# Kernel optimization log

Hardware: AMD Instinct MI355X
Metric: run time of the kernel (lower is better)

Reference implementation:

```python
import jax, jax.numpy as jnp
import numpy as np

B, S = 4, 8192
DIM, H = 1024, 8
C = 2 * H           # num_channels
E = DIM // C        # head_dim = 64
BASE, START, STRIDE = 10.0, 0, 1
CHUNK = 64
EPS = 1e-8
TWO_PI = 2.0 * np.pi


def setup_inputs() -> dict:
    key = jax.random.key(0)
    k1, k2, k3, k4, k5 = jax.random.split(key, 5)
    inputs = jax.random.normal(k1, (B, S, DIM), jnp.float32)
    timestamps = jnp.sort(jax.random.randint(k2, (B, S), 0, 8192, jnp.int32), axis=-1)
    next_timestamps = jnp.sort(jax.random.randint(k3, (B, S), 0, 8192, jnp.int32), axis=-1)
    mask = jnp.ones((B, S), dtype=bool)
    # learned parameters
    Wv = jax.random.normal(k4, (DIM, DIM), jnp.float32) / np.sqrt(DIM)  # proj_v.weight
    gamma_param = jnp.zeros((H,), jnp.float32)
    alpha = jax.random.normal(k5, (C,), jnp.float32) * 0.02
    beta = jnp.ones((C,), jnp.float32)
    return {"inputs": inputs, "Wv": Wv, "gamma_param": gamma_param, "alpha": alpha,
            "beta": beta, "timestamps": timestamps, "next_timestamps": next_timestamps,
            "mask": mask}


def chunkwise_recurrent_attention(q, k, v, decay_steps, mask, chunk):
    # q,k: [B,S,C,2]; v: [B,S,C,E]; decay_steps: [B,S,C]; mask: [B,S] bool
    b, s, c, d = q.shape
    e = v.shape[-1]
    m4 = mask[..., None, None].astype(q.dtype)
    q = q * m4
    k = k * m4
    v = v * m4
    decay = jnp.where(mask[..., None], decay_steps, jnp.ones_like(decay_steps))
    n = s // chunk

    def chunks(x):  # [B,S,...] -> [n,B,L,...]
        return x.reshape(b, n, chunk, *x.shape[2:]).swapaxes(0, 1)

    qc, kc, vc = chunks(q), chunks(k), chunks(v)
    dc = chunks(decay)                       # [n,B,L,C]
    mc = mask.reshape(b, n, chunk).swapaxes(0, 1)
    causal = jnp.tril(jnp.ones((chunk, chunk), q.dtype))

    def step(state, xs):
        qch, kch, vch, dch, mch = xs         # [B,L,C,2],[B,L,C,2],[B,L,C,E],[B,L,C],[B,L]
        prefix = jnp.cumprod(jnp.clip(dch, EPS), axis=1)            # [B,L,C]
        prev = jnp.einsum('blcd,bcde->blce', qch * prefix[..., None], state)
        dmat = prefix[:, :, None, :] / jnp.clip(prefix[:, None, :, :], EPS)  # [B,L,M,C]
        scores = jnp.einsum('blcd,bmcd->blmc', qch, kch)            # [B,L,M,C]
        weights = scores * dmat * causal[None, :, :, None]
        intra = jnp.einsum('blmc,bmce->blce', weights, vch)
        out = (prev + intra) * mch[..., None, None].astype(qch.dtype)
        plast = prefix[:, -1]                                       # [B,C]
        sw = plast[:, None, :] / jnp.clip(prefix, EPS)              # [B,L,C]
        new_state = state * plast[:, :, None, None] + \
            jnp.einsum('blcd,blce->bcde', kch * sw[..., None], vch)
        return new_state, out

    state0 = jnp.zeros((b, c, d, e), q.dtype)
    _, outs = jax.lax.scan(step, state0, (qc, kc, vc, dc, mc))
    return outs.swapaxes(0, 1).reshape(b, s, c, e)


def _forward(inputs, Wv, gamma_param, alpha, beta, timestamps, next_timestamps, mask):
    values = (inputs @ Wv.T).reshape(B, S, C, E)
    scales = jnp.arange(START, START + H * STRIDE, STRIDE, dtype=jnp.float32)
    intervals = jnp.power(BASE, scales).astype(jnp.int32).astype(jnp.float32)  # buffer cast to long
    scale_factor = TWO_PI * jnp.power(1.0 / BASE, scales)
    ts = timestamps.astype(jnp.float32)
    nts = next_timestamps.astype(jnp.float32)
    theta_k = jnp.remainder(ts[..., None], intervals) * scale_factor   # [B,S,H]
    theta_q = jnp.remainder(nts[..., None], intervals) * scale_factor
    key_ = jnp.stack((jnp.cos(theta_k), jnp.sin(theta_k)), axis=-1)    # [B,S,H,2]
    key_ = jnp.concatenate([key_, key_], axis=2)                       # [B,S,C,2]
    cos_q, sin_q = jnp.cos(theta_q), jnp.sin(theta_q)
    query = jnp.concatenate([jnp.stack((sin_q, -cos_q), -1),
                             jnp.stack((cos_q, sin_q), -1)], axis=2)   # [B,S,C,2]
    gamma = jax.nn.sigmoid(gamma_param)
    loggamma = jnp.log(jnp.clip(gamma, 1e-6))
    delta = jnp.clip(nts - ts, 0.0)
    q_decay = jnp.exp(loggamma * (delta[..., None] * scale_factor))    # [B,S,H]
    q_decay = jnp.concatenate([q_decay, q_decay], axis=-1)             # [B,S,C]
    query = query * q_decay[..., None]
    step_delta = jnp.concatenate(
        [jnp.zeros((B, 1), jnp.float32), jnp.clip(ts[:, 1:] - ts[:, :-1], 0.0)], axis=1)
    decay_steps = jnp.exp(loggamma * (step_delta[..., None] * scale_factor))
    decay_steps = jnp.concatenate([decay_steps, decay_steps], axis=-1)  # [B,S,C]
    out = chunkwise_recurrent_attention(query, key_, values, decay_steps, mask, CHUNK)
    out = out * alpha[None, None, :, None] + values * beta[None, None, :, None]
    return out.reshape(B, S, DIM)


def reference(inputs, Wv, gamma_param, alpha, beta, timestamps, next_timestamps, mask):
    return _forward(inputs, Wv, gamma_param, alpha, beta, timestamps, next_timestamps, mask)
```

## Files before the change

kernel.cpp:

```cpp
#include <hip/hip_runtime.h>
#include <stdint.h>

#define SS   8192
#define DIMD 1024
#define NCH  128
#define CC   16
#define EPSF 1e-8f

typedef __bf16 bh;
typedef bh    bhx4 __attribute__((ext_vector_type(4)));
typedef bh    bhx8 __attribute__((ext_vector_type(8)));
typedef float fx4  __attribute__((ext_vector_type(4)));
typedef unsigned int u32x2 __attribute__((ext_vector_type(2)));

#define GLOAD_LDS16(g, l) __builtin_amdgcn_global_load_lds(                    \
    (const __attribute__((address_space(1))) uint32_t*)(g),                    \
    (__attribute__((address_space(3))) uint32_t*)(l), 16, 0, 0)

#define LDSA(p) ((uint32_t)(uintptr_t)(const __attribute__((address_space(3))) char*)(const char*)(p))

#define SB() __builtin_amdgcn_sched_barrier(0)
#define PRE_BAR()  do { SB(); __builtin_amdgcn_s_barrier(); SB();              \
                        __builtin_amdgcn_s_setprio(1); } while (0)
#define POST_BAR() do { __builtin_amdgcn_s_setprio(0); SB();                   \
                        __builtin_amdgcn_s_barrier(); SB(); } while (0)

__global__ __launch_bounds__(256) void cvt_k(const float* __restrict__ src,
                                             bh* __restrict__ dst, int n8) {
    int i = blockIdx.x * 256 + threadIdx.x;
    if (i >= n8) return;
    const float4 a = reinterpret_cast<const float4*>(src)[i * 2];
    const float4 b = reinterpret_cast<const float4*>(src)[i * 2 + 1];
    bhx8 o;
    o[0] = (bh)a.x; o[1] = (bh)a.y; o[2] = (bh)a.z; o[3] = (bh)a.w;
    o[4] = (bh)b.x; o[5] = (bh)b.y; o[6] = (bh)b.z; o[7] = (bh)b.w;
    reinterpret_cast<bhx8*>(dst)[i] = o;
}

template <typename VT>
__global__ __launch_bounds__(512, 2) void gemm256a(const bh* __restrict__ A,
                                                   const bh* __restrict__ Bw,
                                                   VT* __restrict__ C,
                                                   const int* __restrict__ tsp,
                                                   const float* __restrict__ gammap,
                                                   float* __restrict__ Aws,
                                                   float* __restrict__ plastWs) {
    __shared__ __align__(16) char ldsraw[131072];
    const int lb = blockIdx.x;
    const int logical = (lb & 7) * 64 + (lb >> 3);
    const int mt = logical >> 2;
    const int nt = logical & 3;
    const int tid = threadIdx.x, lane = tid & 63, w = tid >> 6;
    const int wm = w >> 2, wn = w & 3;

    fx4 acc[8][4];
#pragma unroll
    for (int i = 0; i < 8; ++i)
#pragma unroll
        for (int j = 0; j < 4; ++j)
#pragma unroll
            for (int r = 0; r < 4; ++r) acc[i][j][r] = 0.f;

    const int kgo = ((tid & 3) ^ ((tid >> 3) & 3)) << 3;
    const bh* gA0 = A  + (size_t)(mt * 256 + (tid >> 2)) * DIMD + kgo;
    const bh* gB0 = Bw + (size_t)(nt * 256 + (tid >> 2)) * DIMD + kgo;

#define STAGE_U(kt, obase, g, h)                                               \
    { char* lp = ldsraw + ((((kt) & 1) * 65536) + (obase) + (h) * 16384) + tid * 16; \
      const bh* gp = (g) + (kt) * 64 + (h) * 32;                               \
      GLOAD_LDS16(gp, lp);                                                     \
      GLOAD_LDS16(gp + 131072, lp + 8192); }

    const int rAb = wm * 128 + (lane & 15);
    const int rBb = wn * 64 + (lane & 15);
    const int s_swz = (lane >> 4) ^ (((lane & 15) >> 1) & 3);
    const int offA = rAb * 64 + s_swz * 16;
    const int offB = rBb * 64 + s_swz * 16;

    STAGE_U(0, 0, gA0, 0); STAGE_U(0, 32768, gB0, 0);
    STAGE_U(0, 0, gA0, 1); STAGE_U(0, 32768, gB0, 1);
    STAGE_U(1, 0, gA0, 0); STAGE_U(1, 32768, gB0, 0);
    STAGE_U(1, 0, gA0, 1); STAGE_U(1, 32768, gB0, 1);
    asm volatile("s_waitcnt vmcnt(8)" ::: "memory");
    SB(); __builtin_amdgcn_s_barrier(); SB();

#pragma unroll 2
    for (int t = 0; t < 16; ++t) {
        const int buf = t & 1;
        const char* pA0 = ldsraw + buf * 65536 + offA;
        const char* pB0 = ldsraw + buf * 65536 + 32768 + offB;
        bhx8 fa[4], fb[4];

#pragma unroll
        for (int i = 0; i < 4; ++i) fa[i] = *reinterpret_cast<const bhx8*>(pA0 + i * 1024);
#pragma unroll
        for (int j = 0; j < 4; ++j) fb[j] = *reinterpret_cast<const bhx8*>(pB0 + j * 1024);
        if (t >= 1 && t <= 14) STAGE_U(t + 1, 0, gA0, 1);
        PRE_BAR();
#pragma unroll
        for (int i = 0; i < 4; ++i)
#pragma unroll
            for (int j = 0; j < 4; ++j)
                acc[i][j] = __builtin_amdgcn_mfma_f32_16x16x32_bf16(fa[i], fb[j], acc[i][j], 0, 0, 0);
        POST_BAR();

#pragma unroll
        for (int i = 0; i < 4; ++i) fa[i] = *reinterpret_cast<const bhx8*>(pA0 + (4 + i) * 1024);
        if (t <= 13) STAGE_U(t + 2, 32768, gB0, 0);
        PRE_BAR();
#pragma unroll
        for (int i = 0; i < 4; ++i)
#pragma unroll
            for (int j = 0; j < 4; ++j)
                acc[4 + i][j] = __builtin_amdgcn_mfma_f32_16x16x32_bf16(fa[i], fb[j], acc[4 + i][j], 0, 0, 0);
        POST_BAR();

#pragma unroll
        for (int i = 0; i < 4; ++i) fa[i] = *reinterpret_cast<const bhx8*>(pA0 + 16384 + i * 1024);
#pragma unroll
        for (int j = 0; j < 4; ++j) fb[j] = *reinterpret_cast<const bhx8*>(pB0 + 16384 + j * 1024);
        if (t <= 13) STAGE_U(t + 2, 0, gA0, 0);
        PRE_BAR();
#pragma unroll
        for (int i = 0; i < 4; ++i)
#pragma unroll
            for (int j = 0; j < 4; ++j)
                acc[i][j] = __builtin_amdgcn_mfma_f32_16x16x32_bf16(fa[i], fb[j], acc[i][j], 0, 0, 0);
        POST_BAR();

#pragma unroll
        for (int i = 0; i < 4; ++i) fa[i] = *reinterpret_cast<const bhx8*>(pA0 + 16384 + (4 + i) * 1024);
        if (t <= 13) STAGE_U(t + 2, 32768, gB0, 1);
        PRE_BAR();
#pragma unroll
        for (int i = 0; i < 4; ++i)
#pragma unroll
            for (int j = 0; j < 4; ++j)
                acc[4 + i][j] = __builtin_amdgcn_mfma_f32_16x16x32_bf16(fa[i], fb[j], acc[4 + i][j], 0, 0, 0);
        __builtin_amdgcn_s_setprio(0);
        if (t < 14)       { asm volatile("s_waitcnt vmcnt(6)" ::: "memory"); }
        else if (t == 14) { asm volatile("s_waitcnt vmcnt(0)" ::: "memory"); }
        SB(); __builtin_amdgcn_s_barrier(); SB();
    }
#undef STAGE_U

    const int r0 = (lane >> 4) * 4;
    const int c0 = lane & 15;
#pragma unroll
    for (int mi = 0; mi < 8; ++mi) {
#pragma unroll
        for (int ni = 0; ni < 4; ++ni) {
            const size_t m = (size_t)(mt * 256 + wm * 128 + mi * 16 + r0);
            const int    n = nt * 256 + wn * 64 + ni * 16 + c0;
#pragma unroll
            for (int r = 0; r < 4; ++r) {
                if constexpr (sizeof(VT) == 2)
                    C[(m + r) * DIMD + n] = (bh)acc[mi][ni][r];
                else
                    C[(m + r) * DIMD + n] = acc[mi][ni][r];
            }
        }
    }

    float* wlds = (float*)ldsraw + w * 256;
    const int b_ = mt >> 5;
    const int j0 = (mt & 31) * 4;
    const int c_ = nt * 4 + wn;
    const int h_ = c_ & 7;
    float iv = 1.f; double invb = 1.0;
    for (int i = 0; i < h_; i++) { iv *= 10.f; invb *= 0.1; }
    const float sf = (float)(6.283185307179586 * invb);
    const float gm = 1.f / (1.f + expf(-gammap[h_]));
    const float lg = logf(fmaxf(gm, 1e-6f));

#pragma unroll
    for (int jl = 0; jl < 2; ++jl) {
        const int jg = j0 + wm * 2 + jl;
        const int sl = jg * 64 + lane;
        const int its = tsp[b_ * SS + sl];
        const int itp = (sl > 0) ? tsp[b_ * SS + sl - 1] : its;
        int dstep = its - itp; if (dstep < 0) dstep = 0;
        const float dec = expf(lg * ((float)dstep * sf));
        float p = fmaxf(dec, EPSF);
#pragma unroll
        for (int off = 1; off < 64; off <<= 1) {
            float o = __shfl_up(p, off, 64);
            if (lane >= off) p *= o;
        }
        const float plast = __shfl(p, 63, 64);
        const float swv = plast / fmaxf(p, EPSF);
        const float tk = fmodf((float)its, iv) * sf;
        wlds[jl * 128 + lane]      = cosf(tk) * swv;
        wlds[jl * 128 + 64 + lane] = sinf(tk) * swv;
        if (lane == 0) plastWs[(size_t)(b_ * CC + c_) * NCH + jg] = plast;
    }
    asm volatile("s_waitcnt lgkmcnt(0)" ::: "memory");

#pragma unroll
    for (int jl = 0; jl < 2; ++jl) {
        const int jg = j0 + wm * 2 + jl;
        float* ab = Aws + ((size_t)(b_ * CC + c_) * NCH + jg) * 128;
        fx4 w0q[4], w1q[4];
        const int gb = ((lane >> 4) << 2);
#pragma unroll
        for (int q = 0; q < 4; ++q) {
            w0q[q] = *reinterpret_cast<const fx4*>(&wlds[jl * 128 + q * 16 + gb]);
            w1q[q] = *reinterpret_cast<const fx4*>(&wlds[jl * 128 + 64 + q * 16 + gb]);
        }
#pragma unroll
        for (int ni = 0; ni < 4; ++ni) {
            float pa0 = 0.f, pa1 = 0.f;
#pragma unroll
            for (int q = 0; q < 4; ++q)
#pragma unroll
                for (int r = 0; r < 4; ++r) {
                    const float av = acc[jl * 4 + q][ni][r];
                    pa0 += w0q[q][r] * av;
                    pa1 += w1q[q][r] * av;
                }
            pa0 += __shfl_xor(pa0, 16, 64); pa0 += __shfl_xor(pa0, 32, 64);
            pa1 += __shfl_xor(pa1, 16, 64); pa1 += __shfl_xor(pa1, 32, 64);
            const int e = ni * 16 + (lane & 15);
            const int grp = lane >> 4;
            if (grp == 0)      ab[e] = pa0;
            else if (grp == 1) ab[64 + e] = pa1;
        }
    }
}

__global__ __launch_bounds__(256) void gemm_k(const float* __restrict__ Ain,
                                              const float* __restrict__ Win,
                                              float* __restrict__ Cout) {
    __shared__ __align__(16) char ldsraw[20480];
    char* ldsA = ldsraw;
    char* ldsB = ldsraw + 10240;
    const int tid = threadIdx.x;
    const int lane = tid & 63;
    const int w = tid >> 6;
    const int wm = w >> 1, wn = w & 1;
    const int bid = blockIdx.x;
// ... 199 lines not shown
        if (lane >= off) p *= o;
    }
    const float ipv = 1.f / fmaxf(p, EPSF);
    const float tk = fmodf((float)its, iv) * sf;
    const float k0 = cosf(tk), k1 = sinf(tk);
    s_b0[w][lane] = k0 * ipv;
    s_b1[w][lane] = k1 * ipv;
    const float tq = fmodf((float)inx, iv) * sf;
    int dq = inx - its; if (dq < 0) dq = 0;
    const float qd = expf(lg * ((float)dq * sf));
    const float sq = sinf(tq), cq = cosf(tq);
    const int r0i = w * 2, r1i = w * 2 + 1;
    s_a0[r0i][lane] = sq * qd * p * al0;  s_a1[r0i][lane] = -cq * qd * p * al0;
    s_a0[r1i][lane] = cq * qd * p * al1;  s_a1[r1i][lane] = sq * qd * p * al1;
    s_st0[r0i][lane] = st00; s_st1[r0i][lane] = st10;
    s_st0[r1i][lane] = st01; s_st1[r1i][lane] = st11;
    asm volatile("s_waitcnt lgkmcnt(0)" ::: "memory");

    fx4 rb0[2][2], rb1[2][2];
#pragma unroll
    for (int ks = 0; ks < 2; ++ks) {
        const int m0 = ks * 32 + (lane >> 4) * 8;
        rb0[ks][0] = *reinterpret_cast<const fx4*>(&s_b0[w][m0]);
        rb0[ks][1] = *reinterpret_cast<const fx4*>(&s_b0[w][m0 + 4]);
        rb1[ks][0] = *reinterpret_cast<const fx4*>(&s_b1[w][m0]);
        rb1[ks][1] = *reinterpret_cast<const fx4*>(&s_b1[w][m0 + 4]);
    }

#pragma unroll
    for (int cc = 0; cc < 2; ++cc) {
        const int reg = w * 2 + cc;
        const int c = h + cc * 8;
        const char* vbase2 = (const char*)&vt[reg][0];

        bhx8 pa[4][2];
#pragma unroll
        for (int mi = 0; mi < 4; ++mi) {
            const int l = mi * 16 + (lane & 15);
            const float a0l = s_a0[reg][l];
            const float a1l = s_a1[reg][l];
#pragma unroll
            for (int ks = 0; ks < 2; ++ks) {
                if (mi * 16 + 16 <= ks * 32) continue;
                const bool full = (mi * 16 >= ks * 32 + 32);
                bhx8 v;
#pragma unroll
                for (int jj = 0; jj < 8; ++jj) {
                    const int m = ks * 32 + (lane >> 4) * 8 + jj;
                    const float b0m = rb0[ks][jj >> 2][jj & 3];
                    const float b1m = rb1[ks][jj >> 2][jj & 3];
                    const float val = a0l * b0m + a1l * b1m;
                    v[jj] = (full || l >= m) ? (bh)val : (bh)0.f;
                }
                pa[mi][ks] = v;
            }
        }

        if (cc == 0) { asm volatile("s_waitcnt vmcnt(8)" ::: "memory"); }
        else         { asm volatile("s_waitcnt vmcnt(0)" ::: "memory"); }

        const uint32_t tb = LDSA(vbase2) + ((lane >> 4) << 8) + ((lane & 15) << 3);
        bhx8 pb[4][2];
#pragma unroll
        for (int ni = 0; ni < 4; ++ni)
#pragma unroll
            for (int ks = 0; ks < 2; ++ks) {
                const uint32_t a2 = tb + ni * 2048 + ks * 1024;
                u32x2 lo, hi;
                asm volatile("ds_read_b64_tr_b16 %0, %2 offset:0\n\t"
                             "ds_read_b64_tr_b16 %1, %2 offset:128"
                             : "=&v"(lo), "=&v"(hi) : "v"(a2));
                union { u32x2 u[2]; bhx8 f; } u_;
                u_.u[0] = lo; u_.u[1] = hi;
                pb[ni][ks] = u_.f;
            }
        asm volatile("s_waitcnt lgkmcnt(0)" ::: "memory");
        SB();

        fx4 acc[4][4];
#pragma unroll
        for (int mi = 0; mi < 4; ++mi)
#pragma unroll
            for (int ni = 0; ni < 4; ++ni)
#pragma unroll
                for (int r = 0; r < 4; ++r) acc[mi][ni][r] = 0.f;
        __builtin_amdgcn_s_setprio(1);
#pragma unroll
        for (int ks = 0; ks < 2; ++ks)
#pragma unroll
            for (int mi = 0; mi < 4; ++mi) {
                if (mi * 16 + 16 <= ks * 32) continue;
#pragma unroll
                for (int ni = 0; ni < 4; ++ni)
                    acc[mi][ni] = __builtin_amdgcn_mfma_f32_16x16x32_bf16(
                        pa[mi][ks], pb[ni][ks], acc[mi][ni], 0, 0, 0);
            }
        __builtin_amdgcn_s_setprio(0);
        SB();

        float st0e[4], st1e[4];
#pragma unroll
        for (int ni = 0; ni < 4; ++ni) {
            st0e[ni] = s_st0[reg][ni * 16 + (lane & 15)];
            st1e[ni] = s_st1[reg][ni * 16 + (lane & 15)];
        }
        const float bev = (cc == 0) ? be0 : be1;
        float* ob = outp + ((size_t)b * SS + (size_t)j * 64) * DIMD + c * 64 + (lane & 15);
#pragma unroll
        for (int mi = 0; mi < 4; ++mi)
#pragma unroll
            for (int r = 0; r < 4; ++r) {
                const int l = mi * 16 + ((lane >> 4) << 2) + r;
                const float a0l = s_a0[reg][l];
                const float a1l = s_a1[reg][l];
#pragma unroll
                for (int ni = 0; ni < 4; ++ni) {
                    const float vv = (float)*reinterpret_cast<const bh*>(
                        vbase2 + ni * 2048 + (mi * 4 + (lane >> 4)) * 128 + r * 32 + ((lane & 15) << 1));
                    const float o = acc[mi][ni][r] + a0l * st0e[ni] + a1l * st1e[ni] + bev * vv;
                    ob[(size_t)l * DIMD + ni * 16] = o;
                }
            }
    }
}

template <typename VT>
__global__ __launch_bounds__(256) void kc_k(const int* __restrict__ ts,
                                            const int* __restrict__ nts,
                                            const float* __restrict__ gammap,
                                            const float* __restrict__ alphap,
                                            const float* __restrict__ betap,
                                            const VT* values,
                                            const float* __restrict__ Sws,
                                            float* outp) {
    __shared__ float vsm[64][64];
    __shared__ float s_p[64], s_ip[64], s_k0[64], s_k1[64], s_q0[64], s_q1[64];
    __shared__ float s_st[128];
    int bid = blockIdx.x;
    int j = bid & 127;
    int c = (bid >> 7) & 15;
    int b = bid >> 11;
    int h = c & 7;
    int tid = threadIdx.x;
    if (tid < 64) {
        int l = tid;
        int s = j * 64 + l;
        float iv = 1.f; double invb = 1.0;
        for (int i = 0; i < h; i++) { iv *= 10.f; invb *= 0.1; }
        float sf = (float)(6.283185307179586 * invb);
        float gp = gammap[h];
        float gm = 1.f / (1.f + expf(-gp));
        float lg = logf(fmaxf(gm, 1e-6f));
// ... 59 lines not shown
#pragma unroll
    for (int i2 = 0; i2 < 4; i2++) {
        float4 vv = *reinterpret_cast<const float4*>(&vsm[l][eg * 16 + i2 * 4]);
        float4 o4;
        const float* vvp = (const float*)&vv;
        float* o4p = (float*)&o4;
#pragma unroll
        for (int r = 0; r < 4; r++) {
            int i = i2 * 4 + r;
            float prevt = pl_ * (q0 * st0[i] + q1 * st1[i]);
            o4p[r] = (prevt + acc[i]) * al + vvp[r] * be;
        }
        *reinterpret_cast<float4*>(ob + i2 * 4) = o4;
    }
}

extern "C" void kernel_launch(void* const* d_in, const int* in_sizes, int n_in,
                              void* d_out, int out_size, void* d_ws, size_t ws_size,
                              hipStream_t stream) {
    const float* inputs = (const float*)d_in[0];
    const float* Wv     = (const float*)d_in[1];
    const float* gammap = (const float*)d_in[2];
    const float* alphap = (const float*)d_in[3];
    const float* betap  = (const float*)d_in[4];
    const int*   ts     = (const int*)d_in[5];
    const int*   nts    = (const int*)d_in[6];
    float* outp = (float*)d_out;
    char* ws = (char*)d_ws;

    float* Aws     = (float*)ws;
    float* plastWs = (float*)(ws + 4194304);
    float* Sws     = (float*)(ws + 4227072);
    const size_t base   = 8421376;
    const size_t abytes = 67108864;
    const size_t wbytes = 2097152;
    const size_t vbytes = 67108864;

    if (ws_size >= base + abytes + wbytes + vbytes) {
        bh* Abf = (bh*)(ws + base);
        bh* Wbf = (bh*)(ws + base + abytes);
        bh* Vbf = (bh*)(ws + base + abytes + wbytes);
        cvt_k<<<16384, 256, 0, stream>>>(inputs, Abf, 4194304);
        cvt_k<<<512, 256, 0, stream>>>(Wv, Wbf, 131072);
        gemm256a<bh><<<512, 512, 0, stream>>>(Abf, Wbf, Vbf, ts, gammap, Aws, plastWs);
        kb_k<<<64, 128, 0, stream>>>(Aws, plastWs, Sws);
        kc2_k<<<1024, 256, 0, stream>>>(ts, nts, gammap, alphap, betap, Vbf, Sws, outp);
    } else if (ws_size >= base + abytes + wbytes) {
        bh* Abf = (bh*)(ws + base);
        bh* Wbf = (bh*)(ws + base + abytes);
        cvt_k<<<16384, 256, 0, stream>>>(inputs, Abf, 4194304);
        cvt_k<<<512, 256, 0, stream>>>(Wv, Wbf, 131072);
        gemm256a<float><<<512, 512, 0, stream>>>(Abf, Wbf, outp, ts, gammap, Aws, plastWs);
        kb_k<<<64, 128, 0, stream>>>(Aws, plastWs, Sws);
        kc_k<float><<<8192, 256, 0, stream>>>(ts, nts, gammap, alphap, betap, outp, Sws, outp);
    } else {
        gemm_k<<<2048, 256, 0, stream>>>(inputs, Wv, outp);
        ka_k<float><<<4096, 64, 0, stream>>>(ts, gammap, outp, Aws, plastWs);
        kb_k<<<64, 128, 0, stream>>>(Aws, plastWs, Sws);
        kc_k<float><<<8192, 256, 0, stream>>>(ts, nts, gammap, alphap, betap, outp, Sws, outp);
    }
}
```

Measured before the change: 171.5 us.

## Overlap decay/weight prologue with GEMM loads and fold beta*v into MFMA

The GEMM kernel's epilogue computed the per-chunk decay prefix products and cos/sin weights after the main loop. That work now runs in the prologue, while the first tile loads are in flight, and writes into a dedicated shared buffer so the staging LDS is not reused. In the output kernel, the per-element beta*v residual was a scalar bf16 LDS read plus FMA per element. It is replaced by extra MFMAs that multiply a scaled identity fragment by the already-loaded transposed V fragments. This adds 16 MFMAs and extra LDS and registers in exchange for fewer scalar LDS reads and a shorter epilogue.

Result: no change. 173.0 us (+0.9%).

```diff
diff --git a/kernel.cpp b/kernel.cpp
--- a/kernel.cpp
+++ b/kernel.cpp
@@ -46,6 +46,7 @@
                                                    float* __restrict__ Aws,
                                                    float* __restrict__ plastWs) {
     __shared__ __align__(16) char ldsraw[131072];
+    __shared__ float wsm[8][256];
     const int lb = blockIdx.x;
     const int logical = (lb & 7) * 64 + (lb >> 3);
     const int mt = logical >> 2;
@@ -77,10 +78,52 @@
     const int offA = rAb * 64 + s_swz * 16;
     const int offB = rBb * 64 + s_swz * 16;
 
+    const int b_  = mt >> 5;
+    const int j0  = (mt & 31) * 4;
+    const int c_  = nt * 4 + wn;
+    const int h_  = c_ & 7;
+    const int jg0 = j0 + wm * 2;
+    const int sl0 = jg0 * 64 + lane;
+    const int sl1 = sl0 + 64;
+    const int its0 = tsp[b_ * SS + sl0];
+    const int itp0 = (sl0 > 0) ? tsp[b_ * SS + sl0 - 1] : its0;
+    const int its1 = tsp[b_ * SS + sl1];
+    const int itp1 = tsp[b_ * SS + sl1 - 1];
+    const float gpv = gammap[h_];
+    SB();
+
     STAGE_U(0, 0, gA0, 0); STAGE_U(0, 32768, gB0, 0);
     STAGE_U(0, 0, gA0, 1); STAGE_U(0, 32768, gB0, 1);
     STAGE_U(1, 0, gA0, 0); STAGE_U(1, 32768, gB0, 0);
     STAGE_U(1, 0, gA0, 1); STAGE_U(1, 32768, gB0, 1);
+
+    {
+        float iv = 1.f; double invb = 1.0;
+        for (int i = 0; i < h_; i++) { iv *= 10.f; invb *= 0.1; }
+        const float sf = (float)(6.283185307179586 * invb);
+        const float gm = 1.f / (1.f + expf(-gpv));
+        const float lg = logf(fmaxf(gm, 1e-6f));
+#pragma unroll
+        for (int jl = 0; jl < 2; ++jl) {
+            const int its = jl ? its1 : its0;
+            const int itp = jl ? itp1 : itp0;
+            int dstep = its - itp; if (dstep < 0) dstep = 0;
+            const float dec = expf(lg * ((float)dstep * sf));
+            float p = fmaxf(dec, EPSF);
+#pragma unroll
+            for (int off = 1; off < 64; off <<= 1) {
+                float o = __shfl_up(p, off, 64);
+                if (lane >= off) p *= o;
+            }
+            const float plast = __shfl(p, 63, 64);
+            const float swv = plast / fmaxf(p, EPSF);
+            const float tk = fmodf((float)its, iv) * sf;
+            wsm[w][jl * 128 + lane]      = cosf(tk) * swv;
+            wsm[w][jl * 128 + 64 + lane] = sinf(tk) * swv;
+            if (lane == 0) plastWs[(size_t)(b_ * CC + c_) * NCH + (jg0 + jl)] = plast;
+        }
+    }
+
     asm volatile("s_waitcnt vmcnt(8)" ::: "memory");
     SB(); __builtin_amdgcn_s_barrier(); SB();
 
@@ -162,50 +205,15 @@
         }
     }
 
-    float* wlds = (float*)ldsraw + w * 256;
-    const int b_ = mt >> 5;
-    const int j0 = (mt & 31) * 4;
-    const int c_ = nt * 4 + wn;
-    const int h_ = c_ & 7;
-    float iv = 1.f; double invb = 1.0;
-    for (int i = 0; i < h_; i++) { iv *= 10.f; invb *= 0.1; }
-    const float sf = (float)(6.283185307179586 * invb);
-    const float gm = 1.f / (1.f + expf(-gammap[h_]));
-    const float lg = logf(fmaxf(gm, 1e-6f));
-
+    const int gb = ((lane >> 4) << 2);
 #pragma unroll
     for (int jl = 0; jl < 2; ++jl) {
-        const int jg = j0 + wm * 2 + jl;
-        const int sl = jg * 64 + lane;
-        const int its = tsp[b_ * SS + sl];
-        const int itp = (sl > 0) ? tsp[b_ * SS + sl - 1] : its;
-        int dstep = its - itp; if (dstep < 0) dstep = 0;
-        const float dec = expf(lg * ((float)dstep * sf));
-        float p = fmaxf(dec, EPSF);
-#pragma unroll
-        for (int off = 1; off < 64; off <<= 1) {
-            float o = __shfl_up(p, off, 64);
-            if (lane >= off) p *= o;
-        }
-        const float plast = __shfl(p, 63, 64);
-        const float swv = plast / fmaxf(p, EPSF);
-        const float tk = fmodf((float)its, iv) * sf;
-        wlds[jl * 128 + lane]      = cosf(tk) * swv;
-        wlds[jl * 128 + 64 + lane] = sinf(tk) * swv;
-        if (lane == 0) plastWs[(size_t)(b_ * CC + c_) * NCH + jg] = plast;
-    }
-    asm volatile("s_waitcnt lgkmcnt(0)" ::: "memory");
-
-#pragma unroll
-    for (int jl = 0; jl < 2; ++jl) {
-        const int jg = j0 + wm * 2 + jl;
-        float* ab = Aws + ((size_t)(b_ * CC + c_) * NCH + jg) * 128;
+        float* ab = Aws + ((size_t)(b_ * CC + c_) * NCH + (jg0 + jl)) * 128;
         fx4 w0q[4], w1q[4];
-        const int gb = ((lane >> 4) << 2);
 #pragma unroll
         for (int q = 0; q < 4; ++q) {
-            w0q[q] = *reinterpret_cast<const fx4*>(&wlds[jl * 128 + q * 16 + gb]);
-            w1q[q] = *reinterpret_cast<const fx4*>(&wlds[jl * 128 + 64 + q * 16 + gb]);
+            w0q[q] = *reinterpret_cast<const fx4*>(&wsm[w][jl * 128 + q * 16 + gb]);
+            w1q[q] = *reinterpret_cast<const fx4*>(&wsm[w][jl * 128 + 64 + q * 16 + gb]);
         }
 #pragma unroll
         for (int ni = 0; ni < 4; ++ni) {
@@ -471,6 +479,7 @@
         const int reg = w * 2 + cc;
         const int c = h + cc * 8;
         const char* vbase2 = (const char*)&vt[reg][0];
+        const float bev = (cc == 0) ? be0 : be1;
 
         bhx8 pa[4][2];
 #pragma unroll
@@ -493,6 +502,17 @@
                 }
                 pa[mi][ks] = v;
             }
+        }
+
+        bhx8 idf[2];
+#pragma unroll
+        for (int me = 0; me < 2; ++me) {
+            bhx8 z;
+#pragma unroll
+            for (int jj = 0; jj < 8; ++jj) z[jj] = (bh)0.f;
+            const int jj = (lane & 15) + me * 16 - (lane >> 4) * 8;
+            if (jj >= 0 && jj < 8) z[jj] = (bh)bev;
+            idf[me] = z;
         }
 
         if (cc == 0) { asm volatile("s_waitcnt vmcnt(8)" ::: "memory"); }
@@ -534,6 +554,14 @@
                     acc[mi][ni] = __builtin_amdgcn_mfma_f32_16x16x32_bf16(
                         pa[mi][ks], pb[ni][ks], acc[mi][ni], 0, 0, 0);
             }
+#pragma unroll
+        for (int mi = 0; mi < 4; ++mi) {
+            const int ks = mi >> 1;
+#pragma unroll
+            for (int ni = 0; ni < 4; ++ni)
+                acc[mi][ni] = __builtin_amdgcn_mfma_f32_16x16x32_bf16(
+                    idf[mi & 1], pb[ni][ks], acc[mi][ni], 0, 0, 0);
+        }
         __builtin_amdgcn_s_setprio(0);
         SB();
 
@@ -543,7 +571,6 @@
             st0e[ni] = s_st0[reg][ni * 16 + (lane & 15)];
             st1e[ni] = s_st1[reg][ni * 16 + (lane & 15)];
         }
-        const float bev = (cc == 0) ? be0 : be1;
         float* ob = outp + ((size_t)b * SS + (size_t)j * 64) * DIMD + c * 64 + (lane & 15);
 #pragma unroll
         for (int mi = 0; mi < 4; ++mi)
@@ -554,9 +581,7 @@
                 const float a1l = s_a1[reg][l];
 #pragma unroll
                 for (int ni = 0; ni < 4; ++ni) {
-                    const float vv = (float)*reinterpret_cast<const bh*>(
-                        vbase2 + ni * 2048 + (mi * 4 + (lane >> 4)) * 128 + r * 32 + ((lane & 15) << 1));
-                    const float o = acc[mi][ni][r] + a0l * st0e[ni] + a1l * st1e[ni] + bev * vv;
+                    const float o = acc[mi][ni][r] + a0l * st0e[ni] + a1l * st1e[ni];
                     ob[(size_t)l * DIMD + ni * 16] = o;
                 }
             }
```

## Fuse fp32-to-bf16 input conversion into GEMM A-tile staging and fold beta into MFMA

Applied to the files above, without the earlier changes.

Removes the separate conversion kernel for the large activation tensor: the GEMM now loads fp32 A tiles into registers, converts them to bf16 and writes them to LDS, software-pipelined two tiles ahead while B still uses direct global-to-LDS loads. This drops a full write and re-read of a 64 MB bf16 copy of the inputs. Separately, the beta*values skip term in kc2_k is folded into the accumulator via extra MFMAs with a scaled identity fragment, which replaces the scalar per-element reads of values. In exchange the GEMM reads twice the A bytes, needs more registers for the in-flight tiles, and the beta term is now multiplied in bf16 precision.

Measured after the change: 174.6 us. No clear change (+1.8%).

```diff
diff --git a/kernel.cpp b/kernel.cpp
--- a/kernel.cpp
+++ b/kernel.cpp
@@ -37,8 +37,12 @@
     reinterpret_cast<bhx8*>(dst)[i] = o;
 }
 
+#define CVT8(v, f0, f1)                                                        \
+    { v[0]=(bh)(f0).x; v[1]=(bh)(f0).y; v[2]=(bh)(f0).z; v[3]=(bh)(f0).w;      \
+      v[4]=(bh)(f1).x; v[5]=(bh)(f1).y; v[6]=(bh)(f1).z; v[7]=(bh)(f1).w; }
+
 template <typename VT>
-__global__ __launch_bounds__(512, 2) void gemm256a(const bh* __restrict__ A,
+__global__ __launch_bounds__(512, 2) void gemm256a(const float* __restrict__ A,
                                                    const bh* __restrict__ Bw,
                                                    VT* __restrict__ C,
                                                    const int* __restrict__ tsp,
@@ -61,15 +65,30 @@
 #pragma unroll
             for (int r = 0; r < 4; ++r) acc[i][j][r] = 0.f;
 
-    const int kgo = ((tid & 3) ^ ((tid >> 3) & 3)) << 3;
-    const bh* gA0 = A  + (size_t)(mt * 256 + (tid >> 2)) * DIMD + kgo;
-    const bh* gB0 = Bw + (size_t)(nt * 256 + (tid >> 2)) * DIMD + kgo;
-
-#define STAGE_U(kt, obase, g, h)                                               \
-    { char* lp = ldsraw + ((((kt) & 1) * 65536) + (obase) + (h) * 16384) + tid * 16; \
-      const bh* gp = (g) + (kt) * 64 + (h) * 32;                               \
-      GLOAD_LDS16(gp, lp);                                                     \
-      GLOAD_LDS16(gp + 131072, lp + 8192); }
+    const int kg8 = ((tid & 3) ^ ((tid >> 3) & 3)) * 8;
+    const float* gAf = A + (size_t)(mt * 256 + (tid >> 2)) * DIMD + kg8;
+    const bh*    gB0 = Bw + (size_t)(nt * 256 + (tid >> 2)) * DIMD + kg8;
+
+#define LDA_ISSUE(KT, H, D, O)                                                 \
+    { const float* gp_ = gAf + (KT) * 64 + (H) * 32;                           \
+      (D)[(O) + 0] = *reinterpret_cast<const float4*>(gp_);                    \
+      (D)[(O) + 1] = *reinterpret_cast<const float4*>(gp_ + 4);                \
+      (D)[(O) + 2] = *reinterpret_cast<const float4*>(gp_ + 128 * DIMD);       \
+      (D)[(O) + 3] = *reinterpret_cast<const float4*>(gp_ + 128 * DIMD + 4); }
+
+#define LDA_WRITE(BUF, H, D, O)                                                \
+    { char* lp_ = ldsraw + ((BUF) * 65536 + (H) * 16384) + tid * 16;           \
+      bhx8 v0_, v1_;                                                           \
+      CVT8(v0_, (D)[(O) + 0], (D)[(O) + 1]);                                   \
+      CVT8(v1_, (D)[(O) + 2], (D)[(O) + 3]);                                   \
+      *reinterpret_cast<bhx8*>(lp_) = v0_;                                     \
+      *reinterpret_cast<bhx8*>(lp_ + 8192) = v1_; }
+
+#define STAGE_B(KT, BUF, H)                                                    \
+    { char* lp_ = ldsraw + ((BUF) * 65536 + 32768 + (H) * 16384) + tid * 16;   \
+      const bh* gp_ = gB0 + (KT) * 64 + (H) * 32;                              \
+      GLOAD_LDS16(gp_, lp_);                                                   \
+      GLOAD_LDS16(gp_ + 131072, lp_ + 8192); }
 
     const int rAb = wm * 128 + (lane & 15);
     const int rBb = wn * 64 + (lane & 15);
@@ -77,72 +96,92 @@
     const int offA = rAb * 64 + s_swz * 16;
     const int offB = rBb * 64 + s_swz * 16;
 
-    STAGE_U(0, 0, gA0, 0); STAGE_U(0, 32768, gB0, 0);
-    STAGE_U(0, 0, gA0, 1); STAGE_U(0, 32768, gB0, 1);
-    STAGE_U(1, 0, gA0, 0); STAGE_U(1, 32768, gB0, 0);
-    STAGE_U(1, 0, gA0, 1); STAGE_U(1, 32768, gB0, 1);
-    asm volatile("s_waitcnt vmcnt(8)" ::: "memory");
-    SB(); __builtin_amdgcn_s_barrier(); SB();
-
-#pragma unroll 2
-    for (int t = 0; t < 16; ++t) {
-        const int buf = t & 1;
-        const char* pA0 = ldsraw + buf * 65536 + offA;
-        const char* pB0 = ldsraw + buf * 65536 + 32768 + offB;
-        bhx8 fa[4], fb[4];
-
-#pragma unroll
-        for (int i = 0; i < 4; ++i) fa[i] = *reinterpret_cast<const bhx8*>(pA0 + i * 1024);
-#pragma unroll
-        for (int j = 0; j < 4; ++j) fb[j] = *reinterpret_cast<const bhx8*>(pB0 + j * 1024);
-        if (t >= 1 && t <= 14) STAGE_U(t + 1, 0, gA0, 1);
-        PRE_BAR();
-#pragma unroll
-        for (int i = 0; i < 4; ++i)
-#pragma unroll
-            for (int j = 0; j < 4; ++j)
-                acc[i][j] = __builtin_amdgcn_mfma_f32_16x16x32_bf16(fa[i], fb[j], acc[i][j], 0, 0, 0);
-        POST_BAR();
-
-#pragma unroll
-        for (int i = 0; i < 4; ++i) fa[i] = *reinterpret_cast<const bhx8*>(pA0 + (4 + i) * 1024);
-        if (t <= 13) STAGE_U(t + 2, 32768, gB0, 0);
-        PRE_BAR();
-#pragma unroll
-        for (int i = 0; i < 4; ++i)
-#pragma unroll
-            for (int j = 0; j < 4; ++j)
-                acc[4 + i][j] = __builtin_amdgcn_mfma_f32_16x16x32_bf16(fa[i], fb[j], acc[4 + i][j], 0, 0, 0);
-        POST_BAR();
-
-#pragma unroll
-        for (int i = 0; i < 4; ++i) fa[i] = *reinterpret_cast<const bhx8*>(pA0 + 16384 + i * 1024);
-#pragma unroll
-        for (int j = 0; j < 4; ++j) fb[j] = *reinterpret_cast<const bhx8*>(pB0 + 16384 + j * 1024);
-        if (t <= 13) STAGE_U(t + 2, 0, gA0, 0);
-        PRE_BAR();
-#pragma unroll
-        for (int i = 0; i < 4; ++i)
-#pragma unroll
-            for (int j = 0; j < 4; ++j)
-                acc[i][j] = __builtin_amdgcn_mfma_f32_16x16x32_bf16(fa[i], fb[j], acc[i][j], 0, 0, 0);
-        POST_BAR();
-
-#pragma unroll
-        for (int i = 0; i < 4; ++i) fa[i] = *reinterpret_cast<const bhx8*>(pA0 + 16384 + (4 + i) * 1024);
-        if (t <= 13) STAGE_U(t + 2, 32768, gB0, 1);
-        PRE_BAR();
-#pragma unroll
-        for (int i = 0; i < 4; ++i)
-#pragma unroll
-            for (int j = 0; j < 4; ++j)
-                acc[4 + i][j] = __builtin_amdgcn_mfma_f32_16x16x32_bf16(fa[i], fb[j], acc[4 + i][j], 0, 0, 0);
-        __builtin_amdgcn_s_setprio(0);
-        if (t < 14)       { asm volatile("s_waitcnt vmcnt(6)" ::: "memory"); }
-        else if (t == 14) { asm volatile("s_waitcnt vmcnt(0)" ::: "memory"); }
+    {
+        float4 p0[8], p1[8];
+        LDA_ISSUE(0, 0, p0, 0); LDA_ISSUE(0, 1, p0, 4);
+        LDA_ISSUE(1, 0, p1, 0); LDA_ISSUE(1, 1, p1, 4);
+        STAGE_B(0, 0, 0); STAGE_B(0, 0, 1);
+        STAGE_B(1, 1, 0); STAGE_B(1, 1, 1);
+        asm volatile("s_waitcnt vmcnt(16)" ::: "memory");
+        LDA_WRITE(0, 0, p0, 0); LDA_WRITE(0, 1, p0, 4);
+        asm volatile("s_waitcnt vmcnt(8)" ::: "memory");
+        LDA_WRITE(1, 0, p1, 0); LDA_WRITE(1, 1, p1, 4);
+        asm volatile("s_waitcnt vmcnt(4)" ::: "memory");
+        asm volatile("s_waitcnt lgkmcnt(0)" ::: "memory");
         SB(); __builtin_amdgcn_s_barrier(); SB();
     }
-#undef STAGE_U
+
+    float4 arA[8], arB[8];
+
+#define TILE(T, BUF, ARI, ARW)                                                 \
+  do {                                                                         \
+    const char* pA0 = ldsraw + (BUF) * 65536 + offA;                           \
+    const char* pB0 = ldsraw + (BUF) * 65536 + 32768 + offB;                   \
+    bhx8 fa[4], fb[4];                                                         \
+                           \
+    _Pragma("unroll")                                                          \
+    for (int i = 0; i < 4; ++i) fa[i] = *reinterpret_cast<const bhx8*>(pA0 + i * 1024); \
+    _Pragma("unroll")                                                          \
+    for (int j = 0; j < 4; ++j) fb[j] = *reinterpret_cast<const bhx8*>(pB0 + j * 1024); \
+    if ((T) <= 13) { LDA_ISSUE((T) + 2, 0, ARI, 0); LDA_ISSUE((T) + 2, 1, ARI, 4); } \
+    PRE_BAR();                                                                 \
+    _Pragma("unroll")                                                          \
+    for (int i = 0; i < 4; ++i)                                                \
+      _Pragma("unroll")                                                        \
+      for (int j = 0; j < 4; ++j)                                              \
+        acc[i][j] = __builtin_amdgcn_mfma_f32_16x16x32_bf16(fa[i], fb[j], acc[i][j], 0, 0, 0); \
+    POST_BAR();                                                                \
+                                  \
+    _Pragma("unroll")                                                          \
+    for (int i = 0; i < 4; ++i) fa[i] = *reinterpret_cast<const bhx8*>(pA0 + (4 + i) * 1024); \
+    if ((T) <= 13) STAGE_B((T) + 2, (BUF), 0);                                 \
+    PRE_BAR();                                                                 \
+    _Pragma("unroll")                                                          \
+    for (int i = 0; i < 4; ++i)                                                \
+      _Pragma("unroll")                                                        \
+      for (int j = 0; j < 4; ++j)                                              \
+        acc[4 + i][j] = __builtin_amdgcn_mfma_f32_16x16x32_bf16(fa[i], fb[j], acc[4 + i][j], 0, 0, 0); \
+    POST_BAR();                                                                \
+                              \
+    _Pragma("unroll")                                                          \
+    for (int i = 0; i < 4; ++i) fa[i] = *reinterpret_cast<const bhx8*>(pA0 + 16384 + i * 1024); \
+    _Pragma("unroll")                                                          \
+    for (int j = 0; j < 4; ++j) fb[j] = *reinterpret_cast<const bhx8*>(pB0 + 16384 + j * 1024); \
+    if ((T) >= 1 && (T) <= 14) LDA_WRITE(1 - (BUF), 0, ARW, 0);                \
+    PRE_BAR();                                                                 \
+    _Pragma("unroll")                                                          \
+    for (int i = 0; i < 4; ++i)                                                \
+      _Pragma("unroll")                                                        \
+      for (int j = 0; j < 4; ++j)                                              \
+        acc[i][j] = __builtin_amdgcn_mfma_f32_16x16x32_bf16(fa[i], fb[j], acc[i][j], 0, 0, 0); \
+    POST_BAR();                                                                \
+                 \
+    _Pragma("unroll")                                                          \
+    for (int i = 0; i < 4; ++i) fa[i] = *reinterpret_cast<const bhx8*>(pA0 + 16384 + (4 + i) * 1024); \
+    if ((T) <= 13) STAGE_B((T) + 2, (BUF), 1);                                 \
+    if ((T) >= 1 && (T) <= 14) LDA_WRITE(1 - (BUF), 1, ARW, 4);                \
+    PRE_BAR();                                                                 \
+    _Pragma("unroll")                                                          \
+    for (int i = 0; i < 4; ++i)                                                \
+      _Pragma("unroll")                                                        \
+      for (int j = 0; j < 4; ++j)                                              \
+        acc[4 + i][j] = __builtin_amdgcn_mfma_f32_16x16x32_bf16(fa[i], fb[j], acc[4 + i][j], 0, 0, 0); \
+    __builtin_amdgcn_s_setprio(0);                                             \
+    if ((T) < 14)       { asm volatile("s_waitcnt vmcnt(12)" ::: "memory"); }  \
+    else if ((T) == 14) { asm volatile("s_waitcnt vmcnt(0)" ::: "memory"); }   \
+    asm volatile("s_waitcnt lgkmcnt(0)" ::: "memory");                         \
+    SB(); __builtin_amdgcn_s_barrier(); SB();                                  \
+  } while (0)
+
+    for (int tt = 0; tt < 8; ++tt) {
+        const int te = tt * 2;
+        TILE(te, 0, arA, arB);
+        TILE(te + 1, 1, arB, arA);
+    }
+#undef TILE
+#undef LDA_ISSUE
+#undef LDA_WRITE
+#undef STAGE_B
 
     const int r0 = (lane >> 4) * 4;
     const int c0 = lane & 15;
@@ -167,6 +206,7 @@
     const int j0 = (mt & 31) * 4;
     const int c_ = nt * 4 + wn;
     const int h_ = c_ & 7;
+    const int jg0 = j0 + wm * 2;
     float iv = 1.f; double invb = 1.0;
     for (int i = 0; i < h_; i++) { iv *= 10.f; invb *= 0.1; }
     const float sf = (float)(6.283185307179586 * invb);
@@ -175,7 +215,7 @@
 
 #pragma unroll
     for (int jl = 0; jl < 2; ++jl) {
-        const int jg = j0 + wm * 2 + jl;
+        const int jg = jg0 + jl;
         const int sl = jg * 64 + lane;
         const int its = tsp[b_ * SS + sl];
         const int itp = (sl > 0) ? tsp[b_ * SS + sl - 1] : its;
@@ -198,7 +238,7 @@
 
 #pragma unroll
     for (int jl = 0; jl < 2; ++jl) {
-        const int jg = j0 + wm * 2 + jl;
+        const int jg = jg0 + jl;
         float* ab = Aws + ((size_t)(b_ * CC + c_) * NCH + jg) * 128;
         fx4 w0q[4], w1q[4];
         const int gb = ((lane >> 4) << 2);
@@ -471,6 +511,7 @@
         const int reg = w * 2 + cc;
         const int c = h + cc * 8;
         const char* vbase2 = (const char*)&vt[reg][0];
+        const float bev = (cc == 0) ? be0 : be1;
 
         bhx8 pa[4][2];
 #pragma unroll
@@ -493,6 +534,17 @@
                 }
                 pa[mi][ks] = v;
             }
+        }
+
+        bhx8 idf[2];
+#pragma unroll
+        for (int me = 0; me < 2; ++me) {
+            bhx8 z;
+#pragma unroll
+            for (int jj = 0; jj < 8; ++jj) z[jj] = (bh)0.f;
+            const int jj = (lane & 15) + me * 16 - (lane >> 4) * 8;
+            if (jj >= 0 && jj < 8) z[jj] = (bh)bev;
+            idf[me] = z;
         }
 
         if (cc == 0) { asm volatile("s_waitcnt vmcnt(8)" ::: "memory"); }
@@ -534,6 +586,14 @@
                     acc[mi][ni] = __builtin_amdgcn_mfma_f32_16x16x32_bf16(
                         pa[mi][ks], pb[ni][ks], acc[mi][ni], 0, 0, 0);
             }
+#pragma unroll
+        for (int mi = 0; mi < 4; ++mi) {
+            const int ks = mi >> 1;
+#pragma unroll
+            for (int ni = 0; ni < 4; ++ni)
+                acc[mi][ni] = __builtin_amdgcn_mfma_f32_16x16x32_bf16(
+                    idf[mi & 1], pb[ni][ks], acc[mi][ni], 0, 0, 0);
+        }
         __builtin_amdgcn_s_setprio(0);
         SB();
 
@@ -543,7 +603,6 @@
             st0e[ni] = s_st0[reg][ni * 16 + (lane & 15)];
             st1e[ni] = s_st1[reg][ni * 16 + (lane & 15)];
         }
-        const float bev = (cc == 0) ? be0 : be1;
         float* ob = outp + ((size_t)b * SS + (size_t)j * 64) * DIMD + c * 64 + (lane & 15);
 #pragma unroll
         for (int mi = 0; mi < 4; ++mi)
@@ -554,9 +613,7 @@
                 const float a1l = s_a1[reg][l];
 #pragma unroll
                 for (int ni = 0; ni < 4; ++ni) {
-                    const float vv = (float)*reinterpret_cast<const bh*>(
-                        vbase2 + ni * 2048 + (mi * 4 + (lane >> 4)) * 128 + r * 32 + ((lane & 15) << 1));
-                    const float o = acc[mi][ni][r] + a0l * st0e[ni] + a1l * st1e[ni] + bev * vv;
+                    const float o = acc[mi][ni][r] + a0l * st0e[ni] + a1l * st1e[ni];
                     ob[(size_t)l * DIMD + ni * 16] = o;
                 }
             }
@@ -682,25 +739,20 @@
     float* plastWs = (float*)(ws + 4194304);
     float* Sws     = (float*)(ws + 4227072);
     const size_t base   = 8421376;
-    const size_t abytes = 67108864;
     const size_t wbytes = 2097152;
     const size_t vbytes = 67108864;
 
-    if (ws_size >= base + abytes + wbytes + vbytes) {
-        bh* Abf = (bh*)(ws + base);
-        bh* Wbf = (bh*)(ws + base + abytes);
-        bh* Vbf = (bh*)(ws + base + abytes + wbytes);
-        cvt_k<<<16384, 256, 0, stream>>>(inputs, Abf, 4194304);
+    if (ws_size >= base + wbytes + vbytes) {
+        bh* Wbf = (bh*)(ws + base);
+        bh* Vbf = (bh*)(ws + base + wbytes);
         cvt_k<<<512, 256, 0, stream>>>(Wv, Wbf, 131072);
-        gemm256a<bh><<<512, 512, 0, stream>>>(Abf, Wbf, Vbf, ts, gammap, Aws, plastWs);
+        gemm256a<bh><<<512, 512, 0, stream>>>(inputs, Wbf, Vbf, ts, gammap, Aws, plastWs);
         kb_k<<<64, 128, 0, stream>>>(Aws, plastWs, Sws);
         kc2_k<<<1024, 256, 0, stream>>>(ts, nts, gammap, alphap, betap, Vbf, Sws, outp);
-    } else if (ws_size >= base + abytes + wbytes) {
-        bh* Abf = (bh*)(ws + base);
-        bh* Wbf = (bh*)(ws + base + abytes);
-        cvt_k<<<16384, 256, 0, stream>>>(inputs, Abf, 4194304);
+    } else if (ws_size >= base + wbytes) {
+        bh* Wbf = (bh*)(ws + base);
         cvt_k<<<512, 256, 0, stream>>>(Wv, Wbf, 131072);
-        gemm256a<float><<<512, 512, 0, stream>>>(Abf, Wbf, outp, ts, gammap, Aws, plastWs);
+        gemm256a<float><<<512, 512, 0, stream>>>(inputs, Wbf, outp, ts, gammap, Aws, plastWs);
         kb_k<<<64, 128, 0, stream>>>(Aws, plastWs, Sws);
         kc_k<float><<<8192, 256, 0, stream>>>(ts, nts, gammap, alphap, betap, outp, Sws, outp);
     } else {
```

## Fuse fp32-to-bf16 input conversion into GEMM via fp32 LDS staging

Applied to the files above, without the earlier changes.

Removes the separate conversion kernel that wrote a bf16 copy of the activation matrix. The GEMM now loads fp32 activations straight into LDS through a triple-buffered A ring, converts them to bf16 in registers before the MFMAs, and steps K in 32-wide tiles instead of 64. This saves a full read plus write pass over the bf16 copy of the inputs, at the cost of twice the A bytes through LDS, twice as many barriers per K, and extra convert instructions in the inner loop.

Measured after the change: 221.2 us. 29.0% more time.

```diff
diff --git a/kernel.cpp b/kernel.cpp
--- a/kernel.cpp
+++ b/kernel.cpp
@@ -37,14 +37,18 @@
     reinterpret_cast<bhx8*>(dst)[i] = o;
 }
 
+#define CVT8(v, f0, f1)                                                        \
+    { v[0]=(bh)(f0).x; v[1]=(bh)(f0).y; v[2]=(bh)(f0).z; v[3]=(bh)(f0).w;      \
+      v[4]=(bh)(f1).x; v[5]=(bh)(f1).y; v[6]=(bh)(f1).z; v[7]=(bh)(f1).w; }
+
 template <typename VT>
-__global__ __launch_bounds__(512, 2) void gemm256a(const bh* __restrict__ A,
-                                                   const bh* __restrict__ Bw,
-                                                   VT* __restrict__ C,
-                                                   const int* __restrict__ tsp,
-                                                   const float* __restrict__ gammap,
-                                                   float* __restrict__ Aws,
-                                                   float* __restrict__ plastWs) {
+__global__ __launch_bounds__(512, 2) void gemm256f3(const float* __restrict__ A,
+                                                    const bh* __restrict__ Bw,
+                                                    VT* __restrict__ C,
+                                                    const int* __restrict__ tsp,
+                                                    const float* __restrict__ gammap,
+                                                    float* __restrict__ Aws,
+                                                    float* __restrict__ plastWs) {
     __shared__ __align__(16) char ldsraw[131072];
     const int lb = blockIdx.x;
     const int logical = (lb & 7) * 64 + (lb >> 3);
@@ -61,41 +65,57 @@
 #pragma unroll
             for (int r = 0; r < 4; ++r) acc[i][j][r] = 0.f;
 
-    const int kgo = ((tid & 3) ^ ((tid >> 3) & 3)) << 3;
-    const bh* gA0 = A  + (size_t)(mt * 256 + (tid >> 2)) * DIMD + kgo;
-    const bh* gB0 = Bw + (size_t)(nt * 256 + (tid >> 2)) * DIMD + kgo;
-
-#define STAGE_U(kt, obase, g, h)                                               \
-    { char* lp = ldsraw + ((((kt) & 1) * 65536) + (obase) + (h) * 16384) + tid * 16; \
-      const bh* gp = (g) + (kt) * 64 + (h) * 32;                               \
-      GLOAD_LDS16(gp, lp);                                                     \
-      GLOAD_LDS16(gp + 131072, lp + 8192); }
-
-    const int rAb = wm * 128 + (lane & 15);
-    const int rBb = wn * 64 + (lane & 15);
-    const int s_swz = (lane >> 4) ^ (((lane & 15) >> 1) & 3);
-    const int offA = rAb * 64 + s_swz * 16;
-    const int offB = rBb * 64 + s_swz * 16;
-
-    STAGE_U(0, 0, gA0, 0); STAGE_U(0, 32768, gB0, 0);
-    STAGE_U(0, 0, gA0, 1); STAGE_U(0, 32768, gB0, 1);
-    STAGE_U(1, 0, gA0, 0); STAGE_U(1, 32768, gB0, 0);
-    STAGE_U(1, 0, gA0, 1); STAGE_U(1, 32768, gB0, 1);
-    asm volatile("s_waitcnt vmcnt(8)" ::: "memory");
+    const float* gAf = A + (size_t)(mt * 256 + (tid >> 3)) * DIMD
+                       + ((tid & 7) ^ ((tid >> 3) & 7)) * 4;
+    const bh* gB0 = Bw + (size_t)(nt * 256 + (tid >> 2)) * DIMD
+                    + ((tid & 3) ^ ((tid >> 3) & 3)) * 8;
+
+#define STAGE_A(KT, AU)                                                        \
+    { char* lp_ = ldsraw + (AU) * 32768 + tid * 16;                            \
+      const float* gp_ = gAf + (size_t)(KT) * 32;                              \
+      GLOAD_LDS16(gp_,          lp_);                                          \
+      GLOAD_LDS16(gp_ + 65536,  lp_ + 8192);                                   \
+      GLOAD_LDS16(gp_ + 131072, lp_ + 16384);                                  \
+      GLOAD_LDS16(gp_ + 196608, lp_ + 24576); }
+
+#define STAGE_B(KT, BB)                                                        \
+    { char* lp_ = ldsraw + 98304 + (BB) * 16384 + tid * 16;                    \
+      const bh* gp_ = gB0 + (size_t)(KT) * 32;                                 \
+      GLOAD_LDS16(gp_,          lp_);                                          \
+      GLOAD_LDS16(gp_ + 131072, lp_ + 8192); }
+
+    const int offA2 = (wm * 128 + (lane & 15)) * 128
+                      + ((((lane >> 4) << 1) ^ (lane & 7)) << 4);
+    const int offB = (wn * 64 + (lane & 15)) * 64
+                     + (((lane >> 4) ^ (((lane & 15) >> 1) & 3)) << 4);
+
+    STAGE_A(0, 0); STAGE_B(0, 0);
+    STAGE_A(1, 1); STAGE_B(1, 1);
+    asm volatile("s_waitcnt vmcnt(6)" ::: "memory");
     SB(); __builtin_amdgcn_s_barrier(); SB();
 
+    int abuf = 0;
 #pragma unroll 2
-    for (int t = 0; t < 16; ++t) {
-        const int buf = t & 1;
-        const char* pA0 = ldsraw + buf * 65536 + offA;
-        const char* pB0 = ldsraw + buf * 65536 + 32768 + offB;
+    for (int t = 0; t < 32; ++t) {
+        const int au = abuf;
+        const int au2 = (au >= 1) ? au - 1 : 2;
+        const int bb = t & 1;
+        const char* pA = ldsraw + au * 32768;
+        const char* pB = ldsraw + 98304 + bb * 16384;
         bhx8 fa[4], fb[4];
 
 #pragma unroll
-        for (int i = 0; i < 4; ++i) fa[i] = *reinterpret_cast<const bhx8*>(pA0 + i * 1024);
-#pragma unroll
-        for (int j = 0; j < 4; ++j) fb[j] = *reinterpret_cast<const bhx8*>(pB0 + j * 1024);
-        if (t >= 1 && t <= 14) STAGE_U(t + 1, 0, gA0, 1);
+        for (int mi = 0; mi < 4; ++mi) {
+            const char* a0 = pA + offA2 + mi * 2048;
+            const float4 q0 = *reinterpret_cast<const float4*>(a0);
+            const float4 q1 = *reinterpret_cast<const float4*>(
+                (const char*)((uintptr_t)a0 ^ 16));
+            CVT8(fa[mi], q0, q1);
+        }
+#pragma unroll
+        for (int ni = 0; ni < 4; ++ni)
+            fb[ni] = *reinterpret_cast<const bhx8*>(pB + offB + ni * 1024);
+        if (t <= 29) STAGE_A(t + 2, au2);
         PRE_BAR();
 #pragma unroll
         for (int i = 0; i < 4; ++i)
@@ -105,32 +125,14 @@
         POST_BAR();
 
 #pragma unroll
-        for (int i = 0; i < 4; ++i) fa[i] = *reinterpret_cast<const bhx8*>(pA0 + (4 + i) * 1024);
-        if (t <= 13) STAGE_U(t + 2, 32768, gB0, 0);
-        PRE_BAR();
-#pragma unroll
-        for (int i = 0; i < 4; ++i)
-#pragma unroll
-            for (int j = 0; j < 4; ++j)
-                acc[4 + i][j] = __builtin_amdgcn_mfma_f32_16x16x32_bf16(fa[i], fb[j], acc[4 + i][j], 0, 0, 0);
-        POST_BAR();
-
-#pragma unroll
-        for (int i = 0; i < 4; ++i) fa[i] = *reinterpret_cast<const bhx8*>(pA0 + 16384 + i * 1024);
-#pragma unroll
-        for (int j = 0; j < 4; ++j) fb[j] = *reinterpret_cast<const bhx8*>(pB0 + 16384 + j * 1024);
-        if (t <= 13) STAGE_U(t + 2, 0, gA0, 0);
-        PRE_BAR();
-#pragma unroll
-        for (int i = 0; i < 4; ++i)
-#pragma unroll
-            for (int j = 0; j < 4; ++j)
-                acc[i][j] = __builtin_amdgcn_mfma_f32_16x16x32_bf16(fa[i], fb[j], acc[i][j], 0, 0, 0);
-        POST_BAR();
-
-#pragma unroll
-        for (int i = 0; i < 4; ++i) fa[i] = *reinterpret_cast<const bhx8*>(pA0 + 16384 + (4 + i) * 1024);
-        if (t <= 13) STAGE_U(t + 2, 32768, gB0, 1);
+        for (int mi = 0; mi < 4; ++mi) {
+            const char* a0 = pA + offA2 + (4 + mi) * 2048;
+            const float4 q0 = *reinterpret_cast<const float4*>(a0);
+            const float4 q1 = *reinterpret_cast<const float4*>(
+                (const char*)((uintptr_t)a0 ^ 16));
+            CVT8(fa[mi], q0, q1);
+        }
+        if (t <= 29) STAGE_B(t + 2, bb);
         PRE_BAR();
 #pragma unroll
         for (int i = 0; i < 4; ++i)
@@ -138,11 +140,13 @@
             for (int j = 0; j < 4; ++j)
                 acc[4 + i][j] = __builtin_amdgcn_mfma_f32_16x16x32_bf16(fa[i], fb[j], acc[4 + i][j], 0, 0, 0);
         __builtin_amdgcn_s_setprio(0);
-        if (t < 14)       { asm volatile("s_waitcnt vmcnt(6)" ::: "memory"); }
-        else if (t == 14) { asm volatile("s_waitcnt vmcnt(0)" ::: "memory"); }
+        if (t < 30)       { asm volatile("s_waitcnt vmcnt(6)" ::: "memory"); }
+        else if (t == 30) { asm volatile("s_waitcnt vmcnt(0)" ::: "memory"); }
         SB(); __builtin_amdgcn_s_barrier(); SB();
-    }
-#undef STAGE_U
+        abuf = (abuf == 2) ? 0 : abuf + 1;
+    }
+#undef STAGE_A
+#undef STAGE_B
 
     const int r0 = (lane >> 4) * 4;
     const int c0 = lane & 15;
@@ -167,6 +171,7 @@
     const int j0 = (mt & 31) * 4;
     const int c_ = nt * 4 + wn;
     const int h_ = c_ & 7;
+    const int jg0 = j0 + wm * 2;
     float iv = 1.f; double invb = 1.0;
     for (int i = 0; i < h_; i++) { iv *= 10.f; invb *= 0.1; }
     const float sf = (float)(6.283185307179586 * invb);
@@ -175,7 +180,7 @@
 
 #pragma unroll
     for (int jl = 0; jl < 2; ++jl) {
-        const int jg = j0 + wm * 2 + jl;
+        const int jg = jg0 + jl;
         const int sl = jg * 64 + lane;
         const int its = tsp[b_ * SS + sl];
         const int itp = (sl > 0) ? tsp[b_ * SS + sl - 1] : its;
@@ -198,7 +203,7 @@
 
 #pragma unroll
     for (int jl = 0; jl < 2; ++jl) {
-        const int jg = j0 + wm * 2 + jl;
+        const int jg = jg0 + jl;
         float* ab = Aws + ((size_t)(b_ * CC + c_) * NCH + jg) * 128;
         fx4 w0q[4], w1q[4];
         const int gb = ((lane >> 4) << 2);
@@ -682,25 +687,20 @@
     float* plastWs = (float*)(ws + 4194304);
     float* Sws     = (float*)(ws + 4227072);
     const size_t base   = 8421376;
-    const size_t abytes = 67108864;
     const size_t wbytes = 2097152;
     const size_t vbytes = 67108864;
 
-    if (ws_size >= base + abytes + wbytes + vbytes) {
-        bh* Abf = (bh*)(ws + base);
-        bh* Wbf = (bh*)(ws + base + abytes);
-        bh* Vbf = (bh*)(ws + base + abytes + wbytes);
-        cvt_k<<<16384, 256, 0, stream>>>(inputs, Abf, 4194304);
+    if (ws_size >= base + wbytes + vbytes) {
+        bh* Wbf = (bh*)(ws + base);
+        bh* Vbf = (bh*)(ws + base + wbytes);
         cvt_k<<<512, 256, 0, stream>>>(Wv, Wbf, 131072);
-        gemm256a<bh><<<512, 512, 0, stream>>>(Abf, Wbf, Vbf, ts, gammap, Aws, plastWs);
+        gemm256f3<bh><<<512, 512, 0, stream>>>(inputs, Wbf, Vbf, ts, gammap, Aws, plastWs);
         kb_k<<<64, 128, 0, stream>>>(Aws, plastWs, Sws);
         kc2_k<<<1024, 256, 0, stream>>>(ts, nts, gammap, alphap, betap, Vbf, Sws, outp);
-    } else if (ws_size >= base + abytes + wbytes) {
-        bh* Abf = (bh*)(ws + base);
-        bh* Wbf = (bh*)(ws + base + abytes);
-        cvt_k<<<16384, 256, 0, stream>>>(inputs, Abf, 4194304);
+    } else if (ws_size >= base + wbytes) {
+        bh* Wbf = (bh*)(ws + base);
         cvt_k<<<512, 256, 0, stream>>>(Wv, Wbf, 131072);
-        gemm256a<float><<<512, 512, 0, stream>>>(Abf, Wbf, outp, ts, gammap, Aws, plastWs);
+        gemm256f3<float><<<512, 512, 0, stream>>>(inputs, Wbf, outp, ts, gammap, Aws, plastWs);
         kb_k<<<64, 128, 0, stream>>>(Aws, plastWs, Sws);
         kc_k<float><<<8192, 256, 0, stream>>>(ts, nts, gammap, alphap, betap, outp, Sws, outp);
     } else {
```
